# Kernel optimization log

Measured on AMD Instinct MI355X. Metric: run time of the kernel, lower is better.

The kernel has to match this reference:

```python
import jax, jax.numpy as jnp
import numpy as np

# Config (matches init_kwargs)
N_PARTS = 4
N_DATASETS = 2
N_VOLUMES = 16
N_TRANSFORMS = 2
TEMP_FAC = 0.1
BS = N_PARTS * N_DATASETS * N_VOLUMES          # 128
N_TOTAL = BS * (N_TRANSFORMS + 1)              # 384 rows in reg_pred
D_FEAT = 131072
PD = N_PARTS * N_DATASETS                      # class period for denominator exclusion
EPS = 1e-6


def setup_inputs() -> dict:
    key = jax.random.key(0)
    reg_pred = jax.random.normal(key, (N_TOTAL, D_FEAT), dtype=jnp.float32)
    return {"reg_pred": reg_pred}


def reference(reg_pred) -> jnp.ndarray:
    # Cosine similarity with torch's eps clamp on each norm.
    norms = jnp.maximum(jnp.linalg.norm(reg_pred, axis=1, keepdims=True), EPS)
    xn = reg_pred / norms                                   # [N, D]
    sims = (xn @ xn.T) / TEMP_FAC                           # [N, N] full cos-sim matrix
    e = jnp.exp(sims)

    # Denominator for pos_index p excludes every column j with j % PD == p % PD
    # (dataset_similar=False, within_dataset=False). Precompute per-class column sums.
    jmod = jnp.arange(N_TOTAL) % PD                          # [N]
    class_sum = jax.ops.segment_sum(e.T, jmod, num_segments=PD).T  # [N, PD]
    row_sum = jnp.sum(e, axis=1)                             # [N]

    p = jnp.arange(BS)
    rem = p % PD
    i1 = p
    i2 = BS + p
    i3 = (p + PD) % N_TOTAL
    i4 = (BS + p + PD) % N_TOTAL
    i5 = 2 * BS + p
    i6 = (2 * BS + p + PD) % N_TOTAL

    def pair_loss(a, b):
        en = e[a, b]                                         # exp(cos(xi,xj)/t), [BS]
        den_a = row_sum[a] - class_sum[a, rem]               # sum exp over den indexes
        den_b = row_sum[b] - class_sum[b, rem]
        return jnp.sum(-jnp.log(en / (en + den_a)) - jnp.log(en / (en + den_b)))

    total = (pair_loss(i1, i2) + pair_loss(i3, i4) + pair_loss(i1, i3)
             + pair_loss(i2, i4) + pair_loss(i5, i6) + pair_loss(i2, i5)
             + pair_loss(i4, i6))
    return total / (N_TRANSFORMS * 3 * BS)
```

## Files before the change

kernel.cpp:

```cpp
#include <hip/hip_runtime.h>
#include <hip/hip_bf16.h>

#define N_TOTAL 384
#define BS 128
#define PD 8
#define D_FEAT 131072
#define EPS 1e-6f

#define NSTRIP 256
#define COLS_PER (D_FEAT / NSTRIP)
#define CHUNK 32
#define NCH (COLS_PER / CHUNK)
#define NSLOT 24

typedef __attribute__((ext_vector_type(4))) float f32x4;
typedef __attribute__((ext_vector_type(8))) __bf16 bf16x8;
typedef __attribute__((ext_vector_type(4))) __bf16 bf16x4;

typedef __attribute__((address_space(1))) const unsigned int gu32;
typedef __attribute__((address_space(3))) unsigned int lu32;

__device__ __forceinline__ void gload16(const void* g, void* l) {
    __builtin_amdgcn_global_load_lds((gu32*)g, (lu32*)l, 16, 0, 0);
}

static __device__ const int SAt[8][3] = {{0,0,0},{0,0,0},{1,1,1},{1,1,1},
                                         {2,2,4},{2,2,4},{3,3,5},{3,3,5}};
static __device__ const int SBt[8][3] = {{0,1,2},{3,4,5},{0,1,2},{3,4,5},
                                         {2,3,4},{4,5,5},{2,3,4},{4,5,5}};
static __device__ const int SRB2[NSLOT] = {0,0,0, 0,0,0, 1,1,1, 1,1,1,
                                           2,2,4, 2,2,4, 3,3,5, 3,3,5};
static __device__ const int SCB2[NSLOT] = {0,1,2, 3,4,5, 0,1,2, 3,4,5,
                                           2,3,4, 4,5,5, 2,3,4, 4,5,5};

__device__ __forceinline__ float gsym(const float* __restrict__ G, int i, int j) {
    return ((i >> 7) <= (j >> 7)) ? G[(size_t)i * N_TOTAL + j]
                                  : G[(size_t)j * N_TOTAL + i];
}

__device__ __forceinline__ bf16x8 fragld(const char* bptr, int row, int kg) {
    const int k = row & 7;
    const f32x4 lo = *(const f32x4*)(bptr + row * 128 + (((2 * kg)     ^ k) * 16));
    const f32x4 hi = *(const f32x4*)(bptr + row * 128 + (((2 * kg + 1) ^ k) * 16));
    bf16x8 r;
    r[0] = (__bf16)lo[0]; r[1] = (__bf16)lo[1]; r[2] = (__bf16)lo[2]; r[3] = (__bf16)lo[3];
    r[4] = (__bf16)hi[0]; r[5] = (__bf16)hi[1]; r[6] = (__bf16)hi[2]; r[7] = (__bf16)hi[3];
    return r;
}

__global__ __launch_bounds__(512) void gram_fused_kernel(const float* __restrict__ X,
                                                         __bf16* __restrict__ P) {
    __shared__ char sm[3][N_TOTAL * 128];

    const int strip = blockIdx.x;
    const int tid  = threadIdx.x;
    const int wave = tid >> 6;
    const int lane = tid & 63;
    const int r16  = lane & 15;
    const int kg   = lane >> 4;

    const int A0 = SAt[wave][0] * 64, A2 = SAt[wave][2] * 64;
    const int B0 = SBt[wave][0] * 64, B1 = SBt[wave][1] * 64, B2 = SBt[wave][2] * 64;

    const int lg = (tid & 7) ^ ((tid >> 3) & 7);
    const char* src0 = (const char*)(X + (size_t)(tid >> 3) * D_FEAT
                                       + (size_t)strip * COLS_PER) + lg * 16;

    f32x4 acc0[4][4], acc1[4][4], acc2[4][4];
#pragma unroll
    for (int m = 0; m < 4; m++)
#pragma unroll
        for (int n = 0; n < 4; n++) {
            acc0[m][n] = (f32x4)(0.0f); acc1[m][n] = (f32x4)(0.0f); acc2[m][n] = (f32x4)(0.0f);
        }

#define STAGE(buf, t)                                                                     \
    _Pragma("unroll") for (int s = 0; s < 6; s++)                                         \
        gload16(src0 + (size_t)s * (64ull * D_FEAT * 4) + (size_t)(t) * 128,              \
                (char*)sm[buf] + s * 8192 + tid * 16);

#define SUBT(accX, Bb)                                                                    \
    do {                                                                                  \
        bf16x8 bf[4];                                                                     \
        _Pragma("unroll") for (int n = 0; n < 4; n++)                                     \
            bf[n] = fragld(bptr, (Bb) + n * 16 + r16, kg);                                \
        _Pragma("unroll") for (int m = 0; m < 4; m++)                                     \
            _Pragma("unroll") for (int n = 0; n < 4; n++)                                 \
                accX[m][n] = __builtin_amdgcn_mfma_f32_16x16x32_bf16(af[m], bf[n],        \
                                                                     accX[m][n], 0, 0, 0);\
    } while (0)

    STAGE(0, 0);
    STAGE(1, 1);

    for (int t = 0; t < NCH; ++t) {
        if (t < NCH - 1) asm volatile("s_waitcnt vmcnt(6)" ::: "memory");
        else             asm volatile("s_waitcnt vmcnt(0)" ::: "memory");
        __builtin_amdgcn_sched_barrier(0);
        __builtin_amdgcn_s_barrier();
        if (t + 2 < NCH) STAGE((t + 2) % 3, t + 2);

        const char* bptr = sm[t % 3];
        bf16x8 af[4];
#pragma unroll
        for (int m = 0; m < 4; m++) af[m] = fragld(bptr, A0 + m * 16 + r16, kg);
        SUBT(acc0, B0);
        SUBT(acc1, B1);
#pragma unroll
        for (int m = 0; m < 4; m++) af[m] = fragld(bptr, A2 + m * 16 + r16, kg);
        SUBT(acc2, B2);
    }
#undef STAGE
#undef SUBT

    const int crow = (lane >> 4) * 4;
    const int ccol = lane & 15;
#define STOREP(accX, s)                                                                   \
    do {                                                                                  \
        __bf16* base = P + ((size_t)strip * NSLOT + wave * 3 + (s)) * 4096;               \
        _Pragma("unroll") for (int m = 0; m < 4; m++)                                     \
            _Pragma("unroll") for (int n = 0; n < 4; n++) {                               \
                bf16x4 v;                                                                 \
                v[0] = (__bf16)accX[m][n][0]; v[1] = (__bf16)accX[m][n][1];               \
                v[2] = (__bf16)accX[m][n][2]; v[3] = (__bf16)accX[m][n][3];               \
                *(bf16x4*)(base + (n * 16 + ccol) * 64 + m * 16 + crow) = v;              \
            }                                                                             \
    } while (0)
    STOREP(acc0, 0);
    STOREP(acc1, 1);
    STOREP(acc2, 2);
#undef STOREP
}

__global__ __launch_bounds__(128) void reduce_kernel(const __bf16* __restrict__ P,
                                                     float* __restrict__ G) {
    const int gidx = blockIdx.x * 128 + threadIdx.x;
    const int slot = gidx >> 11;
    const int pe   = (gidx & 2047) * 2;

    const unsigned* p = (const unsigned*)(P + (size_t)slot * 4096 + pe);
    const size_t stride = (size_t)NSLOT * 4096 / 2;
    float s0 = 0.0f, s1 = 0.0f;
#pragma unroll 16
    for (int strip = 0; strip < NSTRIP; ++strip) {
        const unsigned u = p[stride * strip];
        s0 += __uint_as_float(u << 16);
        s1 += __uint_as_float(u & 0xffff0000u);
    }

    const int rb  = SRB2[slot] * 64;
    const int cb  = SCB2[slot] * 64;
    const int col = pe >> 6;
    const int row = pe & 63;
    G[(size_t)(rb + row)     * N_TOTAL + cb + col] = s0;
    G[(size_t)(rb + row + 1) * N_TOTAL + cb + col] = s1;
}

__global__ __launch_bounds__(128) void den_kernel(const float* __restrict__ G,
                                                  float* __restrict__ den) {
    const int i = blockIdx.x;
    __shared__ float sInv[N_TOTAL];
    for (int j = threadIdx.x; j < N_TOTAL; j += 128) {
        const float n = sqrtf(G[(size_t)j * N_TOTAL + j]);
        sInv[j] = 1.0f / fmaxf(n, EPS);
    }
    __syncthreads();

    const float mi  = sInv[i] * 10.0f;
    const int   myc = i & 7;
    float s = 0.0f;
    for (int j = threadIdx.x; j < N_TOTAL; j += 128) {
        if ((j & 7) != myc)
            s += expf(gsym(G, i, j) * mi * sInv[j]);
    }
#pragma unroll
    for (int off = 32; off > 0; off >>= 1) s += __shfl_down(s, off, 64);
    __shared__ float partial[2];
    if ((threadIdx.x & 63) == 0) partial[threadIdx.x >> 6] = s;
    __syncthreads();
    if (threadIdx.x == 0) den[i] = partial[0] + partial[1];
}

__global__ __launch_bounds__(256) void loss_kernel(const float* __restrict__ G,
                                                   const float* __restrict__ den,
                                                   float* __restrict__ out) {
    __shared__ float sInv[N_TOTAL];
    for (int j = threadIdx.x; j < N_TOTAL; j += 256) {
        const float n = sqrtf(G[(size_t)j * N_TOTAL + j]);
        sInv[j] = 1.0f / fmaxf(n, EPS);
    }
    __syncthreads();

    float s = 0.0f;
    for (int idx = threadIdx.x; idx < 7 * BS; idx += 256) {
        const int p   = idx & (BS - 1);
        const int set = idx >> 7;
        int a, b;
        switch (set) {
            case 0:  a = p;                        b = BS + p;                      break;
            case 1:  a = (p + PD) % N_TOTAL;       b = (BS + p + PD) % N_TOTAL;     break;
            case 2:  a = p;                        b = (p + PD) % N_TOTAL;          break;
            case 3:  a = BS + p;                   b = (BS + p + PD) % N_TOTAL;     break;
            case 4:  a = 2 * BS + p;               b = (2 * BS + p + PD) % N_TOTAL; break;
            case 5:  a = BS + p;                   b = 2 * BS + p;                  break;
            default: a = (BS + p + PD) % N_TOTAL;  b = (2 * BS + p + PD) % N_TOTAL; break;
        }
        const float en = expf(gsym(G, a, b) * sInv[a] * sInv[b] * 10.0f);
        s += log1pf(den[a] / en) + log1pf(den[b] / en);
    }
#pragma unroll
    for (int off = 32; off > 0; off >>= 1) s += __shfl_down(s, off, 64);
    __shared__ float partial[4];
    if ((threadIdx.x & 63) == 0) partial[threadIdx.x >> 6] = s;
    __syncthreads();
    if (threadIdx.x == 0)
        out[0] = (partial[0] + partial[1] + partial[2] + partial[3]) / 768.0f;
}

extern "C" void kernel_launch(void* const* d_in, const int* in_sizes, int n_in,
                              void* d_out, int out_size, void* d_ws, size_t ws_size,
                              hipStream_t stream) {
    (void)in_sizes; (void)n_in; (void)out_size; (void)ws_size;
    const float* X   = (const float*)d_in[0];
    float*       out = (float*)d_out;
    float*       G   = (float*)d_ws;
    float*       den = G + (size_t)N_TOTAL * N_TOTAL;
    __bf16*      P   = (__bf16*)((char*)d_ws + (1u << 20));

    gram_fused_kernel<<<NSTRIP, 512, 0, stream>>>(X, P);
    reduce_kernel<<<384, 128, 0, stream>>>(P, G);
    den_kernel<<<N_TOTAL, 128, 0, stream>>>(G, den);
    loss_kernel<<<1, 256, 0, stream>>>(G, den, out);
}
```

Before: 73.89 us.

## Convert staged fp32 tiles to bf16 in shared memory once per chunk

Before, each wave converted fp32 to bf16 inside every fragment load, so the same elements were converted many times across waves and LDS read traffic was doubled. Now each chunk gets a cooperative fp32→bf16 pass into a separate bf16 LDS buffer, and the MFMA operand loads become single 16-byte bf16 reads. The staging ring shrinks from triple to double buffering, and an extra barrier plus an lgkmcnt wait are added per iteration. The XOR swizzle is dropped, which may cause LDS bank conflicts on the 64-byte-stride bf16 rows, and prefetch depth now depends on the conversion pass finishing.

```diff
diff --git a/kernel.cpp b/kernel.cpp
--- a/kernel.cpp
+++ b/kernel.cpp
@@ -38,19 +38,10 @@
                                   : G[(size_t)j * N_TOTAL + i];
 }
 
-__device__ __forceinline__ bf16x8 fragld(const char* bptr, int row, int kg) {
-    const int k = row & 7;
-    const f32x4 lo = *(const f32x4*)(bptr + row * 128 + (((2 * kg)     ^ k) * 16));
-    const f32x4 hi = *(const f32x4*)(bptr + row * 128 + (((2 * kg + 1) ^ k) * 16));
-    bf16x8 r;
-    r[0] = (__bf16)lo[0]; r[1] = (__bf16)lo[1]; r[2] = (__bf16)lo[2]; r[3] = (__bf16)lo[3];
-    r[4] = (__bf16)hi[0]; r[5] = (__bf16)hi[1]; r[6] = (__bf16)hi[2]; r[7] = (__bf16)hi[3];
-    return r;
-}
-
 __global__ __launch_bounds__(512) void gram_fused_kernel(const float* __restrict__ X,
                                                          __bf16* __restrict__ P) {
-    __shared__ char sm[3][N_TOTAL * 128];
+    __shared__ char smf[2][N_TOTAL * 128];
+    __shared__ char smb[2][N_TOTAL * 64];
 
     const int strip = blockIdx.x;
     const int tid  = threadIdx.x;
@@ -62,9 +53,8 @@
     const int A0 = SAt[wave][0] * 64, A2 = SAt[wave][2] * 64;
     const int B0 = SBt[wave][0] * 64, B1 = SBt[wave][1] * 64, B2 = SBt[wave][2] * 64;
 
-    const int lg = (tid & 7) ^ ((tid >> 3) & 7);
     const char* src0 = (const char*)(X + (size_t)(tid >> 3) * D_FEAT
-                                       + (size_t)strip * COLS_PER) + lg * 16;
+                                       + (size_t)strip * COLS_PER) + (tid & 7) * 16;
 
     f32x4 acc0[4][4], acc1[4][4], acc2[4][4];
 #pragma unroll
@@ -77,13 +67,13 @@
 #define STAGE(buf, t)                                                                     \
     _Pragma("unroll") for (int s = 0; s < 6; s++)                                         \
         gload16(src0 + (size_t)s * (64ull * D_FEAT * 4) + (size_t)(t) * 128,              \
-                (char*)sm[buf] + s * 8192 + tid * 16);
+                (char*)smf[buf] + s * 8192 + tid * 16);
 
 #define SUBT(accX, Bb)                                                                    \
     do {                                                                                  \
         bf16x8 bf[4];                                                                     \
         _Pragma("unroll") for (int n = 0; n < 4; n++)                                     \
-            bf[n] = fragld(bptr, (Bb) + n * 16 + r16, kg);                                \
+            bf[n] = *(const bf16x8*)(bptr + ((Bb) + n * 16 + r16) * 64 + kg * 16);        \
         _Pragma("unroll") for (int m = 0; m < 4; m++)                                     \
             _Pragma("unroll") for (int n = 0; n < 4; n++)                                 \
                 accX[m][n] = __builtin_amdgcn_mfma_f32_16x16x32_bf16(af[m], bf[n],        \
@@ -94,20 +84,42 @@
     STAGE(1, 1);
 
     for (int t = 0; t < NCH; ++t) {
+        const int b = t & 1;
         if (t < NCH - 1) asm volatile("s_waitcnt vmcnt(6)" ::: "memory");
         else             asm volatile("s_waitcnt vmcnt(0)" ::: "memory");
         __builtin_amdgcn_sched_barrier(0);
         __builtin_amdgcn_s_barrier();
-        if (t + 2 < NCH) STAGE((t + 2) % 3, t + 2);
-
-        const char* bptr = sm[t % 3];
+        __builtin_amdgcn_sched_barrier(0);
+
+        {
+            const char* fb = smf[b];
+            char*       bb = smb[b];
+#pragma unroll
+            for (int s = 0; s < 6; s++) {
+                const f32x4 v = *(const f32x4*)(fb + (size_t)s * 8192 + tid * 16);
+                bf16x4 o;
+                o[0] = (__bf16)v[0]; o[1] = (__bf16)v[1];
+                o[2] = (__bf16)v[2]; o[3] = (__bf16)v[3];
+                *(bf16x4*)(bb + (size_t)s * 4096 + tid * 8) = o;
+            }
+        }
+
+        asm volatile("s_waitcnt lgkmcnt(0)" ::: "memory");
+        __builtin_amdgcn_sched_barrier(0);
+        __builtin_amdgcn_s_barrier();
+        __builtin_amdgcn_sched_barrier(0);
+        if (t + 2 < NCH) STAGE(b, t + 2);
+
+        const char* bptr = smb[b];
         bf16x8 af[4];
 #pragma unroll
-        for (int m = 0; m < 4; m++) af[m] = fragld(bptr, A0 + m * 16 + r16, kg);
+        for (int m = 0; m < 4; m++)
+            af[m] = *(const bf16x8*)(bptr + (A0 + m * 16 + r16) * 64 + kg * 16);
         SUBT(acc0, B0);
         SUBT(acc1, B1);
 #pragma unroll
-        for (int m = 0; m < 4; m++) af[m] = fragld(bptr, A2 + m * 16 + r16, kg);
+        for (int m = 0; m < 4; m++)
+            af[m] = *(const bf16x8*)(bptr + (A2 + m * 16 + r16) * 64 + kg * 16);
         SUBT(acc2, B2);
     }
 #undef STAGE
```

Result: slower. 76.24 us (+3.2%).
